# Optimization experiments

Measured on AMD Instinct MI355X. Metric: run time of the kernel, lower is better.

The kernel has to match this reference:

```python
import jax, jax.numpy as jnp
import numpy as np

B, F, V = 64, 256, 128   # groups, frames/group, vecs/group (uniform ragged groups)
CF = 512                 # cross_feature


def setup_inputs() -> dict:
    key = jax.random.key(0)
    ks = jax.random.split(key, 18)
    p = lambda k, s: jax.random.normal(k, s, jnp.float32) * 0.02
    return {
        "metas": jax.random.uniform(ks[0], (B, 5), jnp.float32),
        "meta_indexs": jnp.arange(B),
        "frames": jax.random.normal(ks[1], (B * F, 600), jnp.float32),
        "frame_indexs": jnp.repeat(jnp.arange(B), F),
        "vecs": jax.random.normal(ks[2], (B * V, 768), jnp.float32),
        "vec_indexs": jnp.repeat(jnp.arange(B), V),
        "audios": jax.random.normal(ks[3], (B, 128), jnp.float32),
        "audio_indexs": jnp.arange(B),
        "Wfk": p(ks[4], (CF, 600)), "Wfv": p(ks[5], (CF, 600)),
        "Wvk": p(ks[6], (CF, 768)), "Wvv": p(ks[7], (CF, 768)),
        "Wav": p(ks[8], (CF, 128)),
        "Wff_f": p(ks[9], (2, CF, CF)),
        "Wff_v": p(ks[10], (2, CF, CF)),
        "Wff_a": p(ks[11], (2, CF, CF)),
        "Wout1": p(ks[12], (768, 3 * CF + 3)),
        "Wout2": p(ks[13], (512, 768)),
        "Wout3": p(ks[14], (64, 512)),
        "Wout4": p(ks[15], (1, 64)),
    }


def reference(metas, meta_indexs, frames, frame_indexs, vecs, vec_indexs,
              audios, audio_indexs, Wfk, Wfv, Wvk, Wvv, Wav,
              Wff_f, Wff_v, Wff_a, Wout1, Wout2, Wout3, Wout4):
    # groups are uniform: reshape ragged rows into [B, n, d] (indexes are
    # contiguous repeats per setup_inputs, so the mask-gathers become reshapes)
    b = audios.shape[0]
    fb = frames.reshape(b, -1, frames.shape[-1])   # [B,F,600]
    vb = vecs.reshape(b, -1, vecs.shape[-1])       # [B,V,768]
    relu = jax.nn.relu

    f_k = relu(jnp.einsum('bfd,cd->bfc', fb, Wfk))     # [B,F,CF]
    f_v = relu(jnp.einsum('bfd,cd->bfc', fb, Wfv))
    v_k = relu(jnp.einsum('bvd,cd->bvc', vb, Wvk))     # [B,V,CF]
    v_v = relu(jnp.einsum('bvd,cd->bvc', vb, Wvv))
    a_v = relu(audios @ Wav.T)                         # [B,CF]

    # torch: softmax(mm(k, q)) with no dim on an (N,1) tensor -> dim=1 -> ones,
    # so the initial "attended" queries are plain sums of the value projections.
    f_q_p = f_v.sum(axis=1)                            # [B,CF]
    v_q_p = v_v.sum(axis=1)
    a_q_p = a_v                                        # single audio row

    for i in range(2):
        attn_f = jax.nn.softmax(jnp.einsum('bfc,bc->bf', f_k, v_q_p) / CF, axis=1)
        f_c = jnp.einsum('bf,bfc->bc', attn_f, f_v)
        f_q_n = f_c @ Wff_f[i].T + f_q_p
        attn_v = jax.nn.softmax(jnp.einsum('bvc,bc->bv', v_k, v_q_p) / CF, axis=1)
        v_c = jnp.einsum('bv,bvc->bc', attn_v, v_v)
        v_q_n = v_c @ Wff_v[i].T + v_q_p
        # audio attention is softmax over a single element -> weight 1
        a_q_n = a_v @ Wff_a[i].T + a_q_p
        f_q_p, v_q_p, a_q_p = f_q_n, v_q_n, a_q_n      # dropout is dead code

    mean = a_q_p.mean(axis=1, keepdims=True)
    std = a_q_p.std(axis=1, keepdims=True, ddof=1)     # torch.std is unbiased
    na = (a_q_p - mean) / std

    goal = metas[:, 1:2] / 1500.0
    dura = metas[:, 3:4] - metas[:, 2:3]
    dura = jnp.where(dura > 8000.0, 100.0, dura) / 100.0
    create = metas[:, 4:5] / 5.0

    feats = jnp.concatenate([f_q_p, v_q_p, na, goal, create, dura], axis=1)  # [B,1539]
    h = relu(feats @ Wout1.T)
    h = relu(h @ Wout2.T)
    h = relu(h @ Wout3.T)
    out = jax.nn.sigmoid(h @ Wout4.T)                  # [B,1]
    return out[:, 0]
```

## Files before the change

kernel.cpp:

```cpp
#include <hip/hip_runtime.h>
#include <hip/hip_bf16.h>

typedef __attribute__((ext_vector_type(4))) float f32x4;
typedef __attribute__((ext_vector_type(8))) __bf16 bf16x8;
typedef __attribute__((ext_vector_type(8))) unsigned short us8;
typedef __attribute__((ext_vector_type(4))) unsigned int u32x4;

#define LDS_AS __attribute__((address_space(3)))
#define GLB_AS __attribute__((address_space(1)))

__device__ __forceinline__ unsigned short f2bf(float f) {
    unsigned u = __builtin_bit_cast(unsigned, f);
    return (unsigned short)((u + 0x7FFFu + ((u >> 16) & 1u)) >> 16);
}
__device__ __forceinline__ float bf2f(unsigned short h) {
    return __builtin_bit_cast(float, (unsigned)h << 16);
}
__device__ __forceinline__ void cp16(const void* g, void* l) {
    __builtin_amdgcn_global_load_lds((const GLB_AS unsigned int*)g,
                                     (LDS_AS unsigned int*)l, 16, 0, 0);
}

#define NPREPB 544
#define NTOT 557072
__global__ __launch_bounds__(256) void prep_kernel(
    const float* __restrict__ Wfk, const float* __restrict__ Wfv,
    const float* __restrict__ Wvk, const float* __restrict__ Wvv,
    const float* __restrict__ Wout1, const float* __restrict__ audios, const float* __restrict__ Wav,
    unsigned short* __restrict__ wf, unsigned short* __restrict__ wv,
    float* __restrict__ W1p, float* __restrict__ hacc, float* __restrict__ qz,
    float* __restrict__ a_v, float* __restrict__ a_q_p, float* __restrict__ zbuf)
{
    __shared__ float aud[128];
    const int t = threadIdx.x;
    if (blockIdx.x >= NPREPB) {
        const int b = blockIdx.x - NPREPB;
        if (t < 128) aud[t] = audios[b * 128 + t];
        __syncthreads();
        #pragma unroll
        for (int cc = 0; cc < 2; ++cc) {
            int c = 2 * t + cc;
            const float* wr = Wav + (size_t)c * 128;
            float s = 0.f;
            #pragma unroll
            for (int k4 = 0; k4 < 32; ++k4) {
                f32x4 wvv = *(const f32x4*)(wr + k4 * 4);
                s += wvv[0] * aud[k4 * 4] + wvv[1] * aud[k4 * 4 + 1]
                   + wvv[2] * aud[k4 * 4 + 2] + wvv[3] * aud[k4 * 4 + 3];
            }
            s = s > 0.f ? s : 0.f;
            a_v[b * 512 + c] = s;
            a_q_p[b * 512 + c] = s;
        }
        return;
    }
    for (int i = blockIdx.x * 256 + t; i < NTOT; i += NPREPB * 256) {
        int idx = i;
        if (idx < 77824) {
            int row = idx / 76, k = (idx - row * 76) * 8;
            const float* src = row < 512 ? Wfk + (size_t)row * 600 : Wfv + (size_t)(row - 512) * 600;
            us8 o = {0, 0, 0, 0, 0, 0, 0, 0};
            if (k < 600) {
                f32x4 v0 = *(const f32x4*)(src + k);
                f32x4 v1 = *(const f32x4*)(src + k + 4);
                o[0] = f2bf(v0[0]); o[1] = f2bf(v0[1]); o[2] = f2bf(v0[2]); o[3] = f2bf(v0[3]);
                o[4] = f2bf(v1[0]); o[5] = f2bf(v1[1]); o[6] = f2bf(v1[2]); o[7] = f2bf(v1[3]);
            }
            *(us8*)(wf + (size_t)row * 608 + k) = o;
            continue;
        }
        idx -= 77824;
        if (idx < 98304) {
            int row = idx / 96, k = (idx - row * 96) * 8;
            const float* src = (row < 512 ? Wvk + (size_t)row * 768
                                          : Wvv + (size_t)(row - 512) * 768) + k;
            f32x4 v0 = *(const f32x4*)src;
            f32x4 v1 = *(const f32x4*)(src + 4);
            us8 o = {f2bf(v0[0]), f2bf(v0[1]), f2bf(v0[2]), f2bf(v0[3]),
                     f2bf(v1[0]), f2bf(v1[1]), f2bf(v1[2]), f2bf(v1[3])};
            *(us8*)(wv + (size_t)row * 768 + k) = o;
            continue;
        }
        idx -= 98304;
        if (idx < 344064) {
            int r = idx / 448, k = (idx - r * 448) * 4;
            f32x4 o;
            #pragma unroll
            for (int j = 0; j < 4; ++j) {
                int kk = k + j;
                o[j] = kk < 1539 ? Wout1[(size_t)r * 1539 + kk] : 0.f;
            }
            *(f32x4*)(W1p + (size_t)r * 1792 + k) = o;
            continue;
        }
        idx -= 344064;
        if (idx < 20480) {
            f32x4 z = {0, 0, 0, 0};
            *(f32x4*)(hacc + (size_t)idx * 4) = z;
            continue;
        }
        idx -= 20480;
        if (idx < 16384) {
            f32x4 z = {0, 0, 0, 0};
            *(f32x4*)(qz + (size_t)idx * 4) = z;
            continue;
        }
        idx -= 16384;
        {
            f32x4 z = {0, 0, 0, 0};
            *(f32x4*)(zbuf + (size_t)idx * 4) = z;
        }
    }
}

__global__ __launch_bounds__(256) void gemm_fused(
    const float* __restrict__ Afp, int Kreal, int ktiles,
    const unsigned short* __restrict__ B, int Kp,
    unsigned short* __restrict__ C, float* __restrict__ qout, int gshift,
    const float* __restrict__ zbuf)
{
    __shared__ alignas(16) char lds[2][24576];
    const int t = threadIdx.x;
    const int w = t >> 6, l = t & 63;
    const int nwg = gridDim.x;
    const int swz = (blockIdx.x & 7) * (nwg >> 3) + (blockIdx.x >> 3);
    const int bm = swz >> 3, bn = swz & 7;
    const int m0 = bm << 7, n0 = bn << 7;

    const int arow = t >> 3;
    const int acd = t & 7;
    const int brow = t >> 2, bc0 = (t & 3) << 3;

    const int wr = w >> 1, wc = w & 1;

    const int rA = wr * 64 + (l & 15);
    const int keyA = l & 7;
    const int c2 = (l >> 4) << 1;
    const int pa0 = (c2 ^ keyA) << 2;
    const int pa1 = ((c2 + 1) ^ keyA) << 2;
    const int pBoff = ((wc * 64 + (l & 15)) << 5) + ((l >> 4) << 3);

    auto stage = [&](int buf, int kt) {
        char* base = lds[buf];
        #pragma unroll
        for (int q = 0; q < 4; ++q) {
            int row = q * 32 + arow;
            int sc = acd ^ (row & 7);
            int colf = kt * 32 + sc * 4;
            const float* src = (colf < Kreal)
                ? (Afp + (size_t)(m0 + row) * Kreal + colf) : zbuf;
            cp16(src, base + q * 4096 + w * 1024);
        }
        const unsigned short* gb = B + (size_t)(n0 + brow) * Kp + bc0 + kt * 32;
        cp16(gb, base + 16384 + w * 1024);
        cp16(gb + (size_t)64 * Kp, base + 16384 + 4096 + w * 1024);
    };

    stage(0, 0);
    __syncthreads();

    f32x4 acc[4][4] = {};
    int cur = 0;
    for (int kt = 0; kt < ktiles; ++kt) {
        if (kt + 1 < ktiles) stage(cur ^ 1, kt + 1);
        const float* fA = (const float*)(lds[cur]);
        const unsigned short* sB = (const unsigned short*)(lds[cur] + 16384);
        bf16x8 af[4], bfr[4];
        #pragma unroll
        for (int i = 0; i < 4; ++i) {
            const float* rp = fA + (size_t)(rA + i * 16) * 32;
            f32x4 lo = *(const f32x4*)(rp + pa0);
            f32x4 hi = *(const f32x4*)(rp + pa1);
            us8 o = {f2bf(lo[0]), f2bf(lo[1]), f2bf(lo[2]), f2bf(lo[3]),
                     f2bf(hi[0]), f2bf(hi[1]), f2bf(hi[2]), f2bf(hi[3])};
            af[i] = __builtin_bit_cast(bf16x8, o);
            bfr[i] = *(const bf16x8*)(sB + pBoff + i * 512);
        }
        #pragma unroll
        for (int mi = 0; mi < 4; ++mi)
            #pragma unroll
            for (int ni = 0; ni < 4; ++ni)
                acc[mi][ni] = __builtin_amdgcn_mfma_f32_16x16x32_bf16(af[mi], bfr[ni], acc[mi][ni], 0, 0, 0);
        __syncthreads();
        cur ^= 1;
    }

    const int crow0 = m0 + wr * 64 + ((l >> 4) << 2);
    const int ccol0 = n0 + wc * 64 + (l & 15);
    #pragma unroll
    for (int mi = 0; mi < 4; ++mi)
        #pragma unroll
        for (int ni = 0; ni < 4; ++ni)
            #pragma unroll
            for (int j = 0; j < 4; ++j) {
                float v = acc[mi][ni][j];
                v = v > 0.f ? v : 0.f;
                C[(size_t)(crow0 + mi * 16 + j) * 1024 + (ccol0 + ni * 16)] = f2bf(v);
            }
    if (n0 >= 512) {
        const int g = m0 >> gshift;
        float csum[4];
        #pragma unroll
        for (int ni = 0; ni < 4; ++ni) {
            float s = 0.f;
            #pragma unroll
            for (int mi = 0; mi < 4; ++mi)
                #pragma unroll
                for (int j = 0; j < 4; ++j)
                    s += fmaxf(acc[mi][ni][j], 0.f);
            s += __shfl_xor(s, 16, 64);
            s += __shfl_xor(s, 32, 64);
            csum[ni] = s;
        }
        if (l < 16) {
            #pragma unroll
            for (int ni = 0; ni < 4; ++ni)
                atomicAdd(&qout[g * 512 + (ccol0 - 512) + ni * 16], csum[ni]);
        }
    }
}

__global__ __launch_bounds__(256) void scores_kernel(
    const unsigned short* __restrict__ Cf, const unsigned short* __restrict__ Cv,
    const float* __restrict__ v_q_p, float* __restrict__ sbuf, float* __restrict__ fvz)
{
    const int t = threadIdx.x, bid = blockIdx.x;
    if (bid < 64) {
        f32x4 z = {0, 0, 0, 0};
        ((f32x4*)fvz)[bid * 256 + t] = z;
    }
    const int w = t >> 6, l = t & 63;
    int frame, g, soff;
    const unsigned short* X;
    if (bid < 4096) { frame = bid * 4 + w; g = frame >> 8; X = Cf; soff = 0; }
    else            { frame = (bid - 4096) * 4 + w; g = frame >> 7; X = Cv; soff = 16384; }
    const float* vq = v_q_p + g * 512 + l * 8;
    f32x4 q0 = *(const f32x4*)vq;
    f32x4 q1 = *(const f32x4*)(vq + 4);
    u32x4 u = *(const u32x4*)(X + (size_t)frame * 1024 + l * 8);
    float acc = q0[0] * bf2f((unsigned short)(u[0] & 0xffff)) + q0[1] * bf2f((unsigned short)(u[0] >> 16))
              + q0[2] * bf2f((unsigned short)(u[1] & 0xffff)) + q0[3] * bf2f((unsigned short)(u[1] >> 16))
              + q1[0] * bf2f((unsigned short)(u[2] & 0xffff)) + q1[1] * bf2f((unsigned short)(u[2] >> 16))
              + q1[2] * bf2f((unsigned short)(u[3] & 0xffff)) + q1[3] * bf2f((unsigned short)(u[3] >> 16));
    #pragma unroll
    for (int m = 1; m < 64; m <<= 1) acc += __shfl_xor(acc, m, 64);
    if (l == 0) sbuf[soff + frame] = acc * (1.f / 512.f);
}

__global__ __launch_bounds__(256) void pv_kernel(
    const unsigned short* __restrict__ Cf, const unsigned short* __restrict__ Cv,
    const float* __restrict__ sbuf, float* __restrict__ fc, float* __restrict__ vc)
{
    __shared__ float ws[256];
    __shared__ float red[256];
    const int t = threadIdx.x, bid = blockIdx.x;
    int g, chunk, NF, soff;
    const unsigned short* X;
    float* outp;
    if (bid < 512) { g = bid >> 3; chunk = bid & 7; NF = 256; X = Cf; soff = g * 256; outp = fc; }
    else { int b2 = bid - 512; g = b2 >> 2; chunk = b2 & 3; NF = 128; X = Cv; soff = 16384 + g * 128; outp = vc; }
    float s = (t < NF) ? sbuf[soff + t] : -1e30f;
    red[t] = s;
    __syncthreads();
    for (int st = 128; st > 0; st >>= 1) { if (t < st) red[t] = fmaxf(red[t], red[t + st]); __syncthreads(); }
    float m = red[0];
    __syncthreads();
    float e = (t < NF) ? __expf(s - m) : 0.f;
    ws[t] = e;
    red[t] = e;
    __syncthreads();
    for (int st = 128; st > 0; st >>= 1) { if (t < st) red[t] += red[t + st]; __syncthreads(); }
    float inv = 1.f / red[0];
    const int f0 = g * NF + chunk * 32;
    const unsigned int* q = (const unsigned int*)X + (size_t)f0 * 512 + 256 + t;
    float s0 = 0.f, s1 = 0.f;
    #pragma unroll 4
    for (int f = 0; f < 32; ++f) {
        float a = ws[chunk * 32 + f];
        unsigned u = q[(size_t)f * 512];
        s0 += a * bf2f((unsigned short)(u & 0xffff));
        s1 += a * bf2f((unsigned short)(u >> 16));
    }
    atomicAdd(&outp[g * 512 + 2 * t],     s0 * inv);
    atomicAdd(&outp[g * 512 + 2 * t + 1], s1 * inv);
}

__device__ __forceinline__ void gemv_body(
    const float* __restrict__ X, int ldx, int dorelu,
    const float* __restrict__ W, int ldw, float* __restrict__ Y, int ldy,
    int nc, int kc, int bc)
{
    __shared__ float xs[4096];
    const int t = threadIdx.x;
    #pragma unroll
    for (int j = 0; j < 16; ++j) {
        int idx = t + j * 256;
        float v = X[(size_t)(bc * 32 + (idx >> 7)) * ldx + kc * 128 + (idx & 127)];
        xs[idx] = dorelu ? (v > 0.f ? v : 0.f) : v;
    }
    __syncthreads();
    const int r = t & 63, bg = t >> 6;
    const int row = nc * 64 + r;
    const float* wrow = W + (size_t)row * ldw + kc * 128;
    float acc[8] = {};
    #pragma unroll 8
    for (int k4 = 0; k4 < 32; ++k4) {
        f32x4 wvv = *(const f32x4*)(wrow + k4 * 4);
        #pragma unroll
        for (int bb = 0; bb < 8; ++bb) {
            f32x4 xv = *(const f32x4*)(xs + (bg * 8 + bb) * 128 + k4 * 4);
            acc[bb] += wvv[0] * xv[0] + wvv[1] * xv[1] + wvv[2] * xv[2] + wvv[3] * xv[3];
        }
    }
    #pragma unroll
    for (int bb = 0; bb < 8; ++bb)
        atomicAdd(&Y[(size_t)(bc * 32 + bg * 8 + bb) * ldy + row], acc[bb]);
}

__global__ __launch_bounds__(256) void update_kernel(
    const float* __restrict__ Wff_f, const float* __restrict__ Wff_v, const float* __restrict__ Wff_a,
    int iter, const float* __restrict__ fc, const float* __restrict__ vc, const float* __restrict__ a_v,
    float* __restrict__ f_q_p, float* __restrict__ v_q_p, float* __restrict__ a_q_p)
{
    int id = blockIdx.x;
    const int op = id >> 6; id &= 63;
    const int nc = id & 7, kc = (id >> 3) & 3, bc = id >> 5;
    const float* W = (op == 0 ? Wff_f : op == 1 ? Wff_v : Wff_a) + (size_t)iter * 262144;
    const float* X = op == 0 ? fc : op == 1 ? vc : a_v;
    float* Y = op == 0 ? f_q_p : op == 1 ? v_q_p : a_q_p;
    gemv_body(X, 512, 0, W, 512, Y, 512, nc, kc, bc);
}

__global__ __launch_bounds__(256) void gemvb_kernel(
    const float* __restrict__ X, int ldx, int dorelu,
    const float* __restrict__ W, int ldw, float* __restrict__ Y, int ldy,
    int NC, int KC)
{
    int bid = blockIdx.x;
    const int nc = bid % NC; bid /= NC;
    const int kc = bid % KC;
    const int bc = bid / KC;
    gemv_body(X, ldx, dorelu, W, ldw, Y, ldy, nc, kc, bc);
}

__global__ __launch_bounds__(512) void normfeats_kernel(
    const float* __restrict__ a_q_p, const float* __restrict__ f_q_p, const float* __restrict__ v_q_p,
    const float* __restrict__ metas, float* __restrict__ feats)
{
    __shared__ float red[512];
    const int t = threadIdx.x, b = blockIdx.x;
    float a = a_q_p[b * 512 + t];
    red[t] = a;
    __syncthreads();
    for (int s = 256; s > 0; s >>= 1) { if (t < s) red[t] += red[t + s]; __syncthreads(); }
    float mean = red[0] * (1.f / 512.f);
    __syncthreads();
    float d = a - mean;
    red[t] = d * d;
    __syncthreads();
    for (int s = 256; s > 0; s >>= 1) { if (t < s) red[t] += red[t + s]; __syncthreads(); }
    float sd = sqrtf(red[0] * (1.f / 511.f));
    float* fr = feats + (size_t)b * 1792;
    fr[t]        = f_q_p[b * 512 + t];
    fr[512 + t]  = v_q_p[b * 512 + t];
    fr[1024 + t] = d / sd;
    if (t < 256) {
        float v = 0.f;
        if (t == 0) v = metas[b * 5 + 1] * (1.f / 1500.f);
        else if (t == 1) v = metas[b * 5 + 4] * 0.2f;
        else if (t == 2) {
            float du = metas[b * 5 + 3] - metas[b * 5 + 2];
            v = (du > 8000.f ? 100.f : du) * 0.01f;
        }
        fr[1536 + t] = v;
    }
}

__global__ __launch_bounds__(256) void mlp34_kernel(
    const float* __restrict__ h2acc, const float* __restrict__ W3, const float* __restrict__ W4,
    float* __restrict__ out)
{
    __shared__ float xs[512];
    __shared__ float part[256];
    __shared__ float h3[64];
    const int t = threadIdx.x, b = blockIdx.x;
    {
        float v0 = h2acc[(size_t)b * 512 + t];
        float v1 = h2acc[(size_t)b * 512 + 256 + t];
        xs[t] = v0 > 0.f ? v0 : 0.f;
        xs[256 + t] = v1 > 0.f ? v1 : 0.f;
    }
    __syncthreads();
    const int r = t & 63, q = t >> 6;
    const float* wrow = W3 + (size_t)r * 512 + q * 128;
    float acc = 0.f;
    #pragma unroll 8
    for (int k4 = 0; k4 < 32; ++k4) {
        f32x4 wvv = *(const f32x4*)(wrow + k4 * 4);
        f32x4 xv  = *(const f32x4*)(xs + q * 128 + k4 * 4);
        acc += wvv[0] * xv[0] + wvv[1] * xv[1] + wvv[2] * xv[2] + wvv[3] * xv[3];
    }
    part[t] = acc;
    __syncthreads();
    if (t < 64) {
        float h = part[t] + part[t + 64] + part[t + 128] + part[t + 192];
        h3[t] = h > 0.f ? h : 0.f;
    }
    __syncthreads();
    if (t < 64) {
        float v = h3[t] * W4[t];
        #pragma unroll
        for (int m = 1; m < 64; m <<= 1) v += __shfl_xor(v, m, 64);
        if (t == 0) out[b] = 1.f / (1.f + __expf(-v));
    }
}

extern "C" void kernel_launch(void* const* d_in, const int* in_sizes, int n_in,
                              void* d_out, int out_size, void* d_ws, size_t ws_size,
                              hipStream_t stream)
{
    const float* metas  = (const float*)d_in[0];
    const float* frames = (const float*)d_in[2];
    const float* vecs   = (const float*)d_in[4];
    const float* audios = (const float*)d_in[6];
    const float* Wfk   = (const float*)d_in[8];
    const float* Wfv   = (const float*)d_in[9];
    const float* Wvk   = (const float*)d_in[10];
    const float* Wvv   = (const float*)d_in[11];
    const float* Wav   = (const float*)d_in[12];
    const float* Wff_f = (const float*)d_in[13];
    const float* Wff_v = (const float*)d_in[14];
    const float* Wff_a = (const float*)d_in[15];
    const float* Wout1 = (const float*)d_in[16];
    const float* Wout2 = (const float*)d_in[17];
    const float* Wout3 = (const float*)d_in[18];
    const float* Wout4 = (const float*)d_in[19];
    float* out = (float*)d_out;

    char* p = (char*)d_ws;
    auto alloc = [&](size_t n) { char* r = p; p += (n + 255) & ~(size_t)255; return r; };
    unsigned short* wf  = (unsigned short*)alloc(1024ull * 608 * 2);
    unsigned short* wv  = (unsigned short*)alloc(1024ull * 768 * 2);
    unsigned short* Cf  = (unsigned short*)alloc(16384ull * 1024 * 2);
    unsigned short* Cv  = (unsigned short*)alloc(8192ull * 1024 * 2);
    float* W1p   = (float*)alloc(768ull * 1792 * 4);
    float* feats = (float*)alloc(64ull * 1792 * 4);
    float* qbuf  = (float*)alloc(2ull * 64 * 512 * 4);
    float* f_q_p = qbuf;
    float* v_q_p = qbuf + 64 * 512;
    float* a_q_p = (float*)alloc(64ull * 512 * 4);
    float* a_v   = (float*)alloc(64ull * 512 * 4);
    float* fvc   = (float*)alloc(2ull * 64 * 512 * 4);
    float* fcb   = fvc;
    float* vcb   = fvc + 64 * 512;
    float* hacc  = (float*)alloc(81920ull * 4);
    float* h1acc = hacc;
    float* h2acc = hacc + 64 * 768;
    float* sbuf  = (float*)alloc(24576ull * 4);
    float* zbuf  = (float*)alloc(64ull * 4);

    prep_kernel<<<NPREPB + 64, 256, 0, stream>>>(Wfk, Wfv, Wvk, Wvv, Wout1, audios, Wav,
                                                 wf, wv, W1p, hacc, qbuf, a_v, a_q_p, zbuf);
    gemm_fused<<<1024, 256, 0, stream>>>(frames, 600, 19, wf, 608, Cf, f_q_p, 8, zbuf);
    gemm_fused<<<512, 256, 0, stream>>>(vecs, 768, 24, wv, 768, Cv, v_q_p, 7, zbuf);
    for (int i = 0; i < 2; ++i) {
        scores_kernel<<<6144, 256, 0, stream>>>(Cf, Cv, v_q_p, sbuf, fvc);
        pv_kernel<<<768, 256, 0, stream>>>(Cf, Cv, sbuf, fcb, vcb);
        update_kernel<<<192, 256, 0, stream>>>(Wff_f, Wff_v, Wff_a, i, fcb, vcb, a_v,
                                               f_q_p, v_q_p, a_q_p);
    }
    normfeats_kernel<<<64, 512, 0, stream>>>(a_q_p, f_q_p, v_q_p, metas, feats);
    gemvb_kernel<<<336, 256, 0, stream>>>(feats, 1792, 0, W1p, 1792, h1acc, 768, 12, 14);
    gemvb_kernel<<<96, 256, 0, stream>>>(h1acc, 768, 1, Wout2, 768, h2acc, 512, 8, 6);
    mlp34_kernel<<<64, 256, 0, stream>>>(h2acc, Wout3, Wout4, out);
}
```

Before: 178.1 us.

## Triple-buffer GEMM LDS staging with explicit vmcnt waits and native bf16 converts

Moves the fused GEMM's LDS staging from a double buffer to a triple buffer. Loads now run two k-tiles ahead, and fine-grained s_waitcnt vmcnt counts replace the full __syncthreads drain, so global-to-LDS copies overlap more with MFMA work. It also swaps the hand-written fp32-to-bf16 rounding for native __bf16 casts, which may lower to hardware convert instructions. The cost is 50% more LDS per workgroup, which may reduce occupancy, and the hardcoded vmcnt values are fragile if the number of loads per stage changes.

```diff
diff --git a/kernel.cpp b/kernel.cpp
--- a/kernel.cpp
+++ b/kernel.cpp
@@ -119,7 +119,7 @@
     unsigned short* __restrict__ C, float* __restrict__ qout, int gshift,
     const float* __restrict__ zbuf)
 {
-    __shared__ alignas(16) char lds[2][24576];
+    __shared__ alignas(16) char lds[3][24576];
     const int t = threadIdx.x;
     const int w = t >> 6, l = t & 63;
     const int nwg = gridDim.x;
@@ -140,8 +140,7 @@
     const int pa1 = ((c2 + 1) ^ keyA) << 2;
     const int pBoff = ((wc * 64 + (l & 15)) << 5) + ((l >> 4) << 3);
 
-    auto stage = [&](int buf, int kt) {
-        char* base = lds[buf];
+    auto stage = [&](char* base, int kt) {
         #pragma unroll
         for (int q = 0; q < 4; ++q) {
             int row = q * 32 + arow;
@@ -156,13 +155,25 @@
         cp16(gb + (size_t)64 * Kp, base + 16384 + 4096 + w * 1024);
     };
 
-    stage(0, 0);
-    __syncthreads();
+    stage(lds[0], 0);
+    if (ktiles > 1) stage(lds[1], 1);
 
     f32x4 acc[4][4] = {};
     int cur = 0;
     for (int kt = 0; kt < ktiles; ++kt) {
-        if (kt + 1 < ktiles) stage(cur ^ 1, kt + 1);
+        if (kt + 2 < ktiles) {
+            int b2 = cur + 2; if (b2 >= 3) b2 -= 3;
+            stage(lds[b2], kt + 2);
+            asm volatile("s_waitcnt vmcnt(12)" ::: "memory");
+        } else if (kt + 1 < ktiles) {
+            asm volatile("s_waitcnt vmcnt(6)" ::: "memory");
+        } else {
+            asm volatile("s_waitcnt vmcnt(0)" ::: "memory");
+        }
+        __builtin_amdgcn_sched_barrier(0);
+        __builtin_amdgcn_s_barrier();
+        __builtin_amdgcn_sched_barrier(0);
+
         const float* fA = (const float*)(lds[cur]);
         const unsigned short* sB = (const unsigned short*)(lds[cur] + 16384);
         bf16x8 af[4], bfr[4];
@@ -171,9 +182,12 @@
             const float* rp = fA + (size_t)(rA + i * 16) * 32;
             f32x4 lo = *(const f32x4*)(rp + pa0);
             f32x4 hi = *(const f32x4*)(rp + pa1);
-            us8 o = {f2bf(lo[0]), f2bf(lo[1]), f2bf(lo[2]), f2bf(lo[3]),
-                     f2bf(hi[0]), f2bf(hi[1]), f2bf(hi[2]), f2bf(hi[3])};
-            af[i] = __builtin_bit_cast(bf16x8, o);
+            bf16x8 a;
+            a[0] = (__bf16)lo[0]; a[1] = (__bf16)lo[1];
+            a[2] = (__bf16)lo[2]; a[3] = (__bf16)lo[3];
+            a[4] = (__bf16)hi[0]; a[5] = (__bf16)hi[1];
+            a[6] = (__bf16)hi[2]; a[7] = (__bf16)hi[3];
+            af[i] = a;
             bfr[i] = *(const bf16x8*)(sB + pBoff + i * 512);
         }
         #pragma unroll
@@ -181,8 +195,10 @@
             #pragma unroll
             for (int ni = 0; ni < 4; ++ni)
                 acc[mi][ni] = __builtin_amdgcn_mfma_f32_16x16x32_bf16(af[mi], bfr[ni], acc[mi][ni], 0, 0, 0);
-        __syncthreads();
-        cur ^= 1;
+
+        __builtin_amdgcn_sched_barrier(0);
+        __builtin_amdgcn_s_barrier();
+        cur = (cur == 2) ? 0 : cur + 1;
     }
 
     const int crow0 = m0 + wr * 64 + ((l >> 4) << 2);
```

Result: faster. 172.6 us (-3.1%).

## Pre-convert activations to bf16 in prep and merge both projection GEMMs

Applied to the files above, without the earlier changes.

Moves the fp32-to-bf16 conversion of frames and vecs out of the GEMM inner loop into the prep kernel, so the GEMM stages bf16 tiles directly with a simpler LDS layout. The two projection GEMMs are merged into a single launch, and the loop now uses explicit vmcnt waits and raw barriers instead of __syncthreads. Conversions use hardware bf16 casts. The cost is an extra full write and re-read of the bf16 copies of the activations (about 30 MB of extra traffic) plus larger prep grids.

```diff
diff --git a/kernel.cpp b/kernel.cpp
--- a/kernel.cpp
+++ b/kernel.cpp
@@ -9,27 +9,33 @@
 #define LDS_AS __attribute__((address_space(3)))
 #define GLB_AS __attribute__((address_space(1)))
 
-__device__ __forceinline__ unsigned short f2bf(float f) {
-    unsigned u = __builtin_bit_cast(unsigned, f);
-    return (unsigned short)((u + 0x7FFFu + ((u >> 16) & 1u)) >> 16);
-}
 __device__ __forceinline__ float bf2f(unsigned short h) {
     return __builtin_bit_cast(float, (unsigned)h << 16);
+}
+__device__ __forceinline__ unsigned short f2bf(float f) {
+    return __builtin_bit_cast(unsigned short, (__bf16)f);
+}
+__device__ __forceinline__ us8 cvt8(f32x4 a, f32x4 b) {
+    bf16x8 r;
+    r[0] = (__bf16)a[0]; r[1] = (__bf16)a[1]; r[2] = (__bf16)a[2]; r[3] = (__bf16)a[3];
+    r[4] = (__bf16)b[0]; r[5] = (__bf16)b[1]; r[6] = (__bf16)b[2]; r[7] = (__bf16)b[3];
+    return __builtin_bit_cast(us8, r);
 }
 __device__ __forceinline__ void cp16(const void* g, void* l) {
     __builtin_amdgcn_global_load_lds((const GLB_AS unsigned int*)g,
                                      (LDS_AS unsigned int*)l, 16, 0, 0);
 }
 
-#define NPREPB 544
-#define NTOT 557072
+#define NPREPB 2048
+#define NTOT 2588672
 __global__ __launch_bounds__(256) void prep_kernel(
-    const float* __restrict__ Wfk, const float* __restrict__ Wfv,
-    const float* __restrict__ Wvk, const float* __restrict__ Wvv,
+    const float* __restrict__ frames, const float* __restrict__ Wfk, const float* __restrict__ Wfv,
+    const float* __restrict__ vecs, const float* __restrict__ Wvk, const float* __restrict__ Wvv,
     const float* __restrict__ Wout1, const float* __restrict__ audios, const float* __restrict__ Wav,
-    unsigned short* __restrict__ wf, unsigned short* __restrict__ wv,
+    unsigned short* __restrict__ fbf, unsigned short* __restrict__ wf,
+    unsigned short* __restrict__ vbf, unsigned short* __restrict__ wv,
     float* __restrict__ W1p, float* __restrict__ hacc, float* __restrict__ qz,
-    float* __restrict__ a_v, float* __restrict__ a_q_p, float* __restrict__ zbuf)
+    float* __restrict__ a_v, float* __restrict__ a_q_p)
 {
     __shared__ float aud[128];
     const int t = threadIdx.x;
@@ -56,29 +62,38 @@
     }
     for (int i = blockIdx.x * 256 + t; i < NTOT; i += NPREPB * 256) {
         int idx = i;
+        if (idx < 1245184) {
+            int row = idx / 76, k = (idx - row * 76) * 8;
+            us8 o = {0, 0, 0, 0, 0, 0, 0, 0};
+            if (k < 600) {
+                const float* s = frames + (size_t)row * 600 + k;
+                o = cvt8(*(const f32x4*)s, *(const f32x4*)(s + 4));
+            }
+            *(us8*)(fbf + (size_t)row * 608 + k) = o;
+            continue;
+        }
+        idx -= 1245184;
         if (idx < 77824) {
             int row = idx / 76, k = (idx - row * 76) * 8;
             const float* src = row < 512 ? Wfk + (size_t)row * 600 : Wfv + (size_t)(row - 512) * 600;
             us8 o = {0, 0, 0, 0, 0, 0, 0, 0};
-            if (k < 600) {
-                f32x4 v0 = *(const f32x4*)(src + k);
-                f32x4 v1 = *(const f32x4*)(src + k + 4);
-                o[0] = f2bf(v0[0]); o[1] = f2bf(v0[1]); o[2] = f2bf(v0[2]); o[3] = f2bf(v0[3]);
-                o[4] = f2bf(v1[0]); o[5] = f2bf(v1[1]); o[6] = f2bf(v1[2]); o[7] = f2bf(v1[3]);
-            }
+            if (k < 600) o = cvt8(*(const f32x4*)(src + k), *(const f32x4*)(src + k + 4));
             *(us8*)(wf + (size_t)row * 608 + k) = o;
             continue;
         }
         idx -= 77824;
+        if (idx < 786432) {
+            int row = idx / 96, k = (idx - row * 96) * 8;
+            const float* s = vecs + (size_t)row * 768 + k;
+            *(us8*)(vbf + (size_t)row * 768 + k) = cvt8(*(const f32x4*)s, *(const f32x4*)(s + 4));
+            continue;
+        }
+        idx -= 786432;
         if (idx < 98304) {
             int row = idx / 96, k = (idx - row * 96) * 8;
             const float* src = (row < 512 ? Wvk + (size_t)row * 768
                                           : Wvv + (size_t)(row - 512) * 768) + k;
-            f32x4 v0 = *(const f32x4*)src;
-            f32x4 v1 = *(const f32x4*)(src + 4);
-            us8 o = {f2bf(v0[0]), f2bf(v0[1]), f2bf(v0[2]), f2bf(v0[3]),
-                     f2bf(v1[0]), f2bf(v1[1]), f2bf(v1[2]), f2bf(v1[3])};
-            *(us8*)(wv + (size_t)row * 768 + k) = o;
+            *(us8*)(wv + (size_t)row * 768 + k) = cvt8(*(const f32x4*)src, *(const f32x4*)(src + 4));
             continue;
         }
         idx -= 98304;
@@ -100,88 +115,83 @@
             continue;
         }
         idx -= 20480;
-        if (idx < 16384) {
+        {
             f32x4 z = {0, 0, 0, 0};
             *(f32x4*)(qz + (size_t)idx * 4) = z;
-            continue;
-        }
-        idx -= 16384;
-        {
-            f32x4 z = {0, 0, 0, 0};
-            *(f32x4*)(zbuf + (size_t)idx * 4) = z;
-        }
-    }
-}
-
-__global__ __launch_bounds__(256) void gemm_fused(
-    const float* __restrict__ Afp, int Kreal, int ktiles,
-    const unsigned short* __restrict__ B, int Kp,
-    unsigned short* __restrict__ C, float* __restrict__ qout, int gshift,
-    const float* __restrict__ zbuf)
-{
-    __shared__ alignas(16) char lds[2][24576];
+        }
+    }
+}
+
+__global__ __launch_bounds__(256) void gemm_bt_relu(
+    const unsigned short* __restrict__ Af, const unsigned short* __restrict__ Bf,
+    unsigned short* __restrict__ Cfo, float* __restrict__ qf,
+    const unsigned short* __restrict__ Av, const unsigned short* __restrict__ Bv,
+    unsigned short* __restrict__ Cvo, float* __restrict__ qv)
+{
+    __shared__ alignas(16) unsigned short sA[2][4096];
+    __shared__ alignas(16) unsigned short sB[2][4096];
     const int t = threadIdx.x;
     const int w = t >> 6, l = t & 63;
-    const int nwg = gridDim.x;
-    const int swz = (blockIdx.x & 7) * (nwg >> 3) + (blockIdx.x >> 3);
+    const unsigned short *A, *B;
+    unsigned short* C;
+    float* qout;
+    int Kp, ktiles, gshift, nwg, pb;
+    if (blockIdx.x < 1024) { A = Af; B = Bf; C = Cfo; qout = qf; Kp = 608; ktiles = 19; gshift = 8; nwg = 1024; pb = blockIdx.x; }
+    else                   { A = Av; B = Bv; C = Cvo; qout = qv; Kp = 768; ktiles = 24; gshift = 7; nwg = 512;  pb = blockIdx.x - 1024; }
+    const int swz = (pb & 7) * (nwg >> 3) + (pb >> 3);
     const int bm = swz >> 3, bn = swz & 7;
     const int m0 = bm << 7, n0 = bn << 7;
 
-    const int arow = t >> 3;
-    const int acd = t & 7;
-    const int brow = t >> 2, bc0 = (t & 3) << 3;
+    const int srow = t >> 2, sk0 = (t & 3) << 3;
+    const unsigned short* gA = A + (size_t)(m0 + srow) * Kp + sk0;
+    const unsigned short* gB = B + (size_t)(n0 + srow) * Kp + sk0;
 
     const int wr = w >> 1, wc = w & 1;
-
-    const int rA = wr * 64 + (l & 15);
-    const int keyA = l & 7;
-    const int c2 = (l >> 4) << 1;
-    const int pa0 = (c2 ^ keyA) << 2;
-    const int pa1 = ((c2 + 1) ^ keyA) << 2;
-    const int pBoff = ((wc * 64 + (l & 15)) << 5) + ((l >> 4) << 3);
+    const int fAoff = (wr * 64 + (l & 15)) * 32 + ((l >> 4) << 3);
+    const int fBoff = (wc * 64 + (l & 15)) * 32 + ((l >> 4) << 3);
 
     auto stage = [&](int buf, int kt) {
-        char* base = lds[buf];
-        #pragma unroll
-        for (int q = 0; q < 4; ++q) {
-            int row = q * 32 + arow;
-            int sc = acd ^ (row & 7);
-            int colf = kt * 32 + sc * 4;
-            const float* src = (colf < Kreal)
-                ? (Afp + (size_t)(m0 + row) * Kreal + colf) : zbuf;
-            cp16(src, base + q * 4096 + w * 1024);
-        }
-        const unsigned short* gb = B + (size_t)(n0 + brow) * Kp + bc0 + kt * 32;
-        cp16(gb, base + 16384 + w * 1024);
-        cp16(gb + (size_t)64 * Kp, base + 16384 + 4096 + w * 1024);
+        char* lA = (char*)(&sA[buf][0]) + w * 1024;
+        char* lB = (char*)(&sB[buf][0]) + w * 1024;
+        const unsigned short* ga = gA + kt * 32;
+        const unsigned short* gb = gB + kt * 32;
+        cp16(ga, lA);
+        cp16(ga + (size_t)64 * Kp, lA + 4096);
+        cp16(gb, lB);
+        cp16(gb + (size_t)64 * Kp, lB + 4096);
     };
 
     stage(0, 0);
-    __syncthreads();
-
     f32x4 acc[4][4] = {};
     int cur = 0;
     for (int kt = 0; kt < ktiles; ++kt) {
-        if (kt + 1 < ktiles) stage(cur ^ 1, kt + 1);
-        const float* fA = (const float*)(lds[cur]);
-        const unsigned short* sB = (const unsigned short*)(lds[cur] + 16384);
+        if (kt + 1 < ktiles) {
+            stage(cur ^ 1, kt + 1);
+            asm volatile("s_waitcnt vmcnt(4)" ::: "memory");
+        } else {
+            asm volatile("s_waitcnt vmcnt(0)" ::: "memory");
+        }
+        __builtin_amdgcn_sched_barrier(0);
+        __builtin_amdgcn_s_barrier();
+        __builtin_amdgcn_sched_barrier(0);
+
         bf16x8 af[4], bfr[4];
         #pragma unroll
         for (int i = 0; i < 4; ++i) {
-            const float* rp = fA + (size_t)(rA + i * 16) * 32;
-            f32x4 lo = *(const f32x4*)(rp + pa0);
-            f32x4 hi = *(const f32x4*)(rp + pa1);
-            us8 o = {f2bf(lo[0]), f2bf(lo[1]), f2bf(lo[2]), f2bf(lo[3]),
-                     f2bf(hi[0]), f2bf(hi[1]), f2bf(hi[2]), f2bf(hi[3])};
-            af[i] = __builtin_bit_cast(bf16x8, o);
-            bfr[i] = *(const bf16x8*)(sB + pBoff + i * 512);
+            af[i]  = *(const bf16x8*)(&sA[cur][0] + fAoff + i * 512);
+            bfr[i] = *(const bf16x8*)(&sB[cur][0] + fBoff + i * 512);
         }
         #pragma unroll
         for (int mi = 0; mi < 4; ++mi)
             #pragma unroll
             for (int ni = 0; ni < 4; ++ni)
                 acc[mi][ni] = __builtin_amdgcn_mfma_f32_16x16x32_bf16(af[mi], bfr[ni], acc[mi][ni], 0, 0, 0);
-        __syncthreads();
+
+        if (kt + 1 < ktiles) {
+            asm volatile("s_waitcnt lgkmcnt(0)" ::: "memory");
+            __builtin_amdgcn_sched_barrier(0);
+            __builtin_amdgcn_s_barrier();
+        }
         cur ^= 1;
     }
 
@@ -439,7 +449,9 @@
 
     char* p = (char*)d_ws;
     auto alloc = [&](size_t n) { char* r = p; p += (n + 255) & ~(size_t)255; return r; };
+    unsigned short* fbf = (unsigned short*)alloc(16384ull * 608 * 2);
     unsigned short* wf  = (unsigned short*)alloc(1024ull * 608 * 2);
+    unsigned short* vbf = (unsigned short*)alloc(8192ull * 768 * 2);
     unsigned short* wv  = (unsigned short*)alloc(1024ull * 768 * 2);
     unsigned short* Cf  = (unsigned short*)alloc(16384ull * 1024 * 2);
     unsigned short* Cv  = (unsigned short*)alloc(8192ull * 1024 * 2);
@@ -457,12 +469,11 @@
     float* h1acc = hacc;
     float* h2acc = hacc + 64 * 768;
     float* sbuf  = (float*)alloc(24576ull * 4);
-    float* zbuf  = (float*)alloc(64ull * 4);
-
-    prep_kernel<<<NPREPB + 64, 256, 0, stream>>>(Wfk, Wfv, Wvk, Wvv, Wout1, audios, Wav,
-                                                 wf, wv, W1p, hacc, qbuf, a_v, a_q_p, zbuf);
-    gemm_fused<<<1024, 256, 0, stream>>>(frames, 600, 19, wf, 608, Cf, f_q_p, 8, zbuf);
-    gemm_fused<<<512, 256, 0, stream>>>(vecs, 768, 24, wv, 768, Cv, v_q_p, 7, zbuf);
+
+    prep_kernel<<<NPREPB + 64, 256, 0, stream>>>(frames, Wfk, Wfv, vecs, Wvk, Wvv, Wout1,
+                                                 audios, Wav, fbf, wf, vbf, wv, W1p, hacc,
+                                                 qbuf, a_v, a_q_p);
+    gemm_bt_relu<<<1536, 256, 0, stream>>>(fbf, wf, Cf, f_q_p, vbf, wv, Cv, v_q_p);
     for (int i = 0; i < 2; ++i) {
         scores_kernel<<<6144, 256, 0, stream>>>(Cf, Cv, v_q_p, sbuf, fvc);
         pv_kernel<<<768, 256, 0, stream>>>(Cf, Cv, sbuf, fcb, vcb);
```

Result: no change. 176.2 us (-1.1%).
